# Kernel tuning notes

Measured on AMD Instinct MI355X. Metric: run time of the kernel, lower is better.

Reference implementation:

```python
import jax, jax.numpy as jnp
import numpy as np

B, A = 64, 32            # graphs, atoms per graph
N, E = B * A, B * A * A  # nodes, fully-connected edges (incl. self-loops)
H, LAT = 512, 256        # hidden_dim, latent_dim
L = 4                    # num CSP layers
NF = 10                  # sinusoid frequencies -> dis_dim = 2*NF*3 = 60
MAXA = 100
DIS = 2 * NF * 3
EIN = 2 * H + 9 + DIS    # edge_mlp input width = 1093


def _lin(k, fan_in, shape):
    return jax.random.normal(k, shape, jnp.float32) * (1.0 / np.sqrt(fan_in))


def setup_inputs() -> dict:
    key = jax.random.key(0)
    ks = jax.random.split(key, 20)
    t = jax.random.normal(ks[0], (B, LAT), jnp.float32)
    atom_types = jax.random.randint(ks[1], (N,), 1, MAXA + 1, dtype=jnp.int32)
    frac_coords = jax.random.uniform(ks[2], (N, 3), jnp.float32)
    lattices = jax.random.normal(ks[3], (B, 3, 3), jnp.float32)
    node2graph = jnp.repeat(jnp.arange(B, dtype=jnp.int32), A)
    # fc edges per graph, row-major like dense_to_sparse(block_diag(ones))
    base = (np.arange(B, dtype=np.int64) * A)[:, None]
    ii = np.repeat(np.arange(A), A)
    jj = np.tile(np.arange(A), A)
    src = (base + ii[None, :]).reshape(-1)
    dst = (base + jj[None, :]).reshape(-1)
    edge_index = jnp.asarray(np.stack([src, dst]), dtype=jnp.int32)
    params = dict(
        emb_table=jax.random.normal(ks[4], (MAXA, H), jnp.float32),
        W_latent=_lin(ks[5], H + LAT, (H + LAT, H)), b_latent=jnp.zeros((H,), jnp.float32),
        edge_W1=_lin(ks[6], EIN, (L, EIN, H)), edge_b1=jnp.zeros((L, H), jnp.float32),
        edge_W2=_lin(ks[7], H, (L, H, H)), edge_b2=jnp.zeros((L, H), jnp.float32),
        node_W1=_lin(ks[8], 2 * H, (L, 2 * H, H)), node_b1=jnp.zeros((L, H), jnp.float32),
        node_W2=_lin(ks[9], H, (L, H, H)), node_b2=jnp.zeros((L, H), jnp.float32),
        coord_W=_lin(ks[10], H, (H, 3)),
        lattice_W=_lin(ks[11], H, (H, 9)),
    )
    return dict(t=t, frac_coords=frac_coords, lattices=lattices, **params,
                atom_types=atom_types, node2graph=node2graph, edge_index=edge_index)


def reference(t, frac_coords, lattices, emb_table, W_latent, b_latent,
              edge_W1, edge_b1, edge_W2, edge_b2,
              node_W1, node_b1, node_W2, node_b2,
              coord_W, lattice_W, atom_types, node2graph, edge_index):
    silu = jax.nn.silu
    src, dst = edge_index[0], edge_index[1]
    edge2graph = node2graph[src]
    # gen_edges (fc): frac_diff per edge
    frac_diff = (frac_coords[dst] - frac_coords[src]) % 1.0            # [E,3]
    # SinusoidsEmbedding (same for every layer)
    freqs = 2.0 * jnp.pi * jnp.arange(NF, dtype=jnp.float32)
    fd = (frac_diff[:, :, None] * freqs).reshape(-1, 3 * NF)
    fd_emb = jnp.concatenate([jnp.sin(fd), jnp.cos(fd)], axis=-1)      # [E,60]
    # lattice inner products (ip=True), broadcast to edges
    lat_ip = jnp.einsum('bij,bkj->bik', lattices, lattices).reshape(-1, 9)
    lat_e = lat_ip[edge2graph]                                          # [E,9]
    # node embedding + time conditioning
    nf = emb_table[atom_types - 1]                                      # [N,H]
    nf = jnp.concatenate([nf, t[node2graph]], axis=1) @ W_latent + b_latent
    ones_e = jnp.ones((src.shape[0], 1), nf.dtype)
    for i in range(L):
        hi, hj = nf[src], nf[dst]
        ein = jnp.concatenate([hi, hj, lat_e, fd_emb], axis=1)          # [E,1093]
        ef = silu(silu(ein @ edge_W1[i] + edge_b1[i]) @ edge_W2[i] + edge_b2[i])
        agg = jax.ops.segment_sum(ef, src, num_segments=N)
        deg = jax.ops.segment_sum(ones_e, src, num_segments=N)
        agg = agg / jnp.maximum(deg, 1.0)                               # scatter-mean
        nin = jnp.concatenate([nf, agg], axis=1)                        # [N,2H]
        nf = nf + silu(silu(nin @ node_W1[i] + node_b1[i]) @ node_W2[i] + node_b2[i])
    coord_out = nf @ coord_W                                            # [N,3]
    gf = jax.ops.segment_sum(nf, node2graph, num_segments=B) / A        # graph mean
    lattice_out = (gf @ lattice_W).reshape(-1, 3, 3)
    lattice_out = jnp.einsum('bij,bjk->bik', lattice_out, lattices)     # ip=True
    return (lattice_out, coord_out)
```

## Files before the change

### kernel.cpp

```cpp
#include <hip/hip_runtime.h>
#include <math.h>


typedef short bf16x8 __attribute__((ext_vector_type(8)));
typedef float f32x4 __attribute__((ext_vector_type(4)));

__device__ __forceinline__ float silu_f(float x) {
    float e = __builtin_amdgcn_exp2f(x * -1.44269504088896f);
    return x * __builtin_amdgcn_rcpf(1.0f + e);
}
__device__ __forceinline__ unsigned short f2bf(float x) {
    unsigned int u = __float_as_uint(x);
    u += 0x7fffu + ((u >> 16) & 1u);
    return (unsigned short)(u >> 16);
}
__device__ __forceinline__ unsigned int cvt_pk_bf16(float lo, float hi) {
    unsigned int r;
    asm("v_cvt_pk_bf16_f32 %0, %1, %2" : "=v"(r) : "v"(lo), "v"(hi));
    return r;
}
__device__ __forceinline__ size_t apack_idx(int ng, int m, int c) {
    return ((size_t)(ng*16 + (c >> 5))*64 + (m + 16*((c >> 3) & 3)))*8 + (c & 7);
}

#define NF_OFF    0
#define UP_OFF    (2048*512)
#define VTD_OFF   (2*2048*512)
#define NFP_OFF   (VTD_OFF + 1048576)
#define H1P_OFF   (NFP_OFF + 524288)
#define AGGP_OFF  (H1P_OFF + 524288)
#define WBF_OFF   (AGGP_OFF + 524288)
#define SZ_INITT (512*768)
#define SZ_UVT   (1024*512)
#define SZ_W1DT  (512*64)
#define SZ_W2T   (512*512)
#define SZ_NW1T  (512*1024)
#define SZ_NW2T  (512*512)
#define SZ_LAYER (SZ_UVT+SZ_W1DT+SZ_W2T+SZ_NW1T+SZ_NW2T)
#define WBF_FLOATS ((SZ_INITT + 4*SZ_LAYER + 1)/2)
#define FDP_OFF   (WBF_OFF + WBF_FLOATS)

__global__ __launch_bounds__(256) void k_prep(
    const float* __restrict__ Wl, const float* __restrict__ eW1,
    const float* __restrict__ eW2, const float* __restrict__ nW1,
    const float* __restrict__ nW2, unsigned short* __restrict__ wbf)
{
    __shared__ float tile[32][33];
    int bid = blockIdx.x;
    const float* src; int K; unsigned short* dst; int t;
    if (bid < 384) { src = Wl; K = 768; dst = wbf; t = bid; }
    else {
        int b = bid - 384; int l = b / 1568; int j = b - l * 1568;
        const float* e1 = eW1 + (size_t)l * 1093 * 512;
        unsigned short* base = wbf + SZ_INITT + (size_t)l * SZ_LAYER;
        if (j < 256)      { src = e1;                       K = 512;  dst = base;                                   t = j; }
        else if (j < 512) { src = e1 + 512*512;             K = 512;  dst = base + 512*512;                         t = j-256; }
        else if (j < 544) { src = e1 + 1033*512;            K = 60;   dst = base + SZ_UVT;                          t = j-512; }
        else if (j < 800) { src = eW2 + (size_t)l*512*512;  K = 512;  dst = base + SZ_UVT+SZ_W1DT;                  t = j-544; }
        else if (j <1312) { src = nW1 + (size_t)l*1024*512; K = 1024; dst = base + SZ_UVT+SZ_W1DT+SZ_W2T;           t = j-800; }
        else              { src = nW2 + (size_t)l*512*512;  K = 512;  dst = base + SZ_UVT+SZ_W1DT+SZ_W2T+SZ_NW1T;   t = j-1312; }
    }
    int tr = t >> 4, tc = t & 15;
    int k0 = tr * 32, nn0 = tc * 32;
    {
        int r8 = threadIdx.x >> 5, cc = threadIdx.x & 31;
        #pragma unroll
        for (int rr = 0; rr < 4; ++rr) {
            int row = rr*8 + r8;
            int k = k0 + row;
            tile[row][cc] = (k < K) ? src[(size_t)k*512 + nn0 + cc] : 0.f;
        }
    }
    __syncthreads();
    int nt_loc = threadIdx.x >> 7;
    int l = (threadIdx.x >> 1) & 63;
    int jh = threadIdx.x & 1;
    int lj = l & 15, lh = l >> 4;
    float v0 = tile[lh*8 + jh*4 + 0][nt_loc*16 + lj];
    float v1 = tile[lh*8 + jh*4 + 1][nt_loc*16 + lj];
    float v2 = tile[lh*8 + jh*4 + 2][nt_loc*16 + lj];
    float v3 = tile[lh*8 + jh*4 + 3][nt_loc*16 + lj];
    uint2 pk = { cvt_pk_bf16(v0, v1), cvt_pk_bf16(v2, v3) };
    *(uint2*)&dst[((size_t)(tr*32 + tc*2 + nt_loc)*64 + l)*8 + jh*4] = pk;
}

__global__ __launch_bounds__(64) void k_fd(const float* __restrict__ frac,
                                           unsigned short* __restrict__ fdP)
{
    int bid = blockIdx.x;
    int n0 = bid * 2, g = n0 >> 5;
    int l = threadIdx.x, lj = l & 15, lh = l >> 4;
    float di[2][2][3];
    #pragma unroll
    for (int h = 0; h < 2; ++h)
        #pragma unroll
        for (int dd = 0; dd < 2; ++dd) {
            int dstn = g*32 + dd*16 + lj;
            #pragma unroll
            for (int comp = 0; comp < 3; ++comp) {
                float d = frac[dstn*3 + comp] - frac[(n0+h)*3 + comp];
                d -= floorf(d);
                di[h][dd][comp] = d;
            }
        }
    #pragma unroll
    for (int kt = 0; kt < 2; ++kt)
        #pragma unroll
        for (int mt = 0; mt < 4; ++mt) {
            int h = mt >> 1, dd = mt & 1;
            unsigned int w[4];
            #pragma unroll
            for (int p = 0; p < 4; ++p) {
                float vv[2];
                #pragma unroll
                for (int e = 0; e < 2; ++e) {
                    int k = kt*32 + lh*8 + p*2 + e;
                    float val = 0.f;
                    if (k < 60) {
                        int isCos = k >= 30;
                        int dq = k - (isCos ? 30 : 0);
                        int comp = dq >= 20 ? 2 : (dq >= 10 ? 1 : 0);
                        int f = dq - comp*10;
                        float u = di[h][dd][comp] * (float)f;
                        u -= floorf(u);
                        val = isCos ? __builtin_amdgcn_cosf(u) : __builtin_amdgcn_sinf(u);
                    }
                    vv[e] = val;
                }
                w[p] = cvt_pk_bf16(vv[0], vv[1]);
            }
            uint4 pk = { w[0], w[1], w[2], w[3] };
            *(uint4*)&fdP[(((size_t)bid*8 + kt*4 + mt)*64 + l)*8] = pk;
        }
}

__global__ __launch_bounds__(256) void k_init(
    const float* __restrict__ tvec, const float* __restrict__ emb,
    const unsigned short* __restrict__ WT, const float* __restrict__ bl,
    const int* __restrict__ atom_types, float* __restrict__ nf,
    unsigned short* __restrict__ nfP)
{
    __shared__ __align__(16) unsigned short cat_s[16*768];
    int ng = blockIdx.x >> 1, half = blockIdx.x & 1;
    int n0 = ng * 16, tid = threadIdx.x;
    for (int idx = tid; idx < 16*192; idx += 256) {
        int m = idx / 192, q = idx - m * 192;
        int k4 = q * 4, n = n0 + m;
        float4 v;
        if (k4 < 512) v = *(const float4*)&emb[(size_t)(atom_types[n]-1)*512 + k4];
        else          v = *(const float4*)&tvec[(size_t)(n>>5)*256 + (k4-512)];
        uint2 pk = { cvt_pk_bf16(v.x, v.y), cvt_pk_bf16(v.z, v.w) };
        *(uint2*)&cat_s[m*768 + (k4 ^ ((m&7)<<3))] = pk;
    }
    __syncthreads();
    int w = tid >> 6, l = tid & 63, lj = l & 15, lh = l >> 4;
    f32x4 acc[4];
    #pragma unroll
    for (int nt = 0; nt < 4; ++nt) acc[nt] = (f32x4){0.f,0.f,0.f,0.f};
    for (int kt = 0; kt < 24; ++kt) {
        int k = kt*32 + lh*8;
        bf16x8 a = *(const bf16x8*)&cat_s[lj*768 + (k ^ ((lj&7)<<3))];
        #pragma unroll
        for (int nt = 0; nt < 4; ++nt) {
            bf16x8 b = *(const bf16x8*)&WT[(((size_t)kt*32 + half*16 + w*4 + nt)*64 + l)*8];
            acc[nt] = __builtin_amdgcn_mfma_f32_16x16x32_bf16(a, b, acc[nt], 0, 0, 0);
        }
    }
    #pragma unroll
    for (int nt = 0; nt < 4; ++nt) {
        int c = half*256 + w*64 + nt*16 + lj;
        float bv = bl[c];
        #pragma unroll
        for (int r = 0; r < 4; ++r) {
            int m = lh*4 + r;
            float v = acc[nt][r] + bv;
            nf[(size_t)(n0 + m)*512 + c] = v;
            nfP[apack_idx(ng, m, c)] = f2bf(v);
        }
    }
}

__global__ __launch_bounds__(256) void k_uv(
    const unsigned short* __restrict__ nfP, const unsigned short* __restrict__ WT,
    const float* __restrict__ lat, const float* __restrict__ W1c,
    const float* __restrict__ b1, float* __restrict__ Up,
    float* __restrict__ VTD)
{
    int ng = blockIdx.x >> 2, half = (blockIdx.x >> 1) & 1, ch = blockIdx.x & 1;
    int n0 = ng * 16, g = n0 >> 5, tid = threadIdx.x;
    int w = tid >> 6, l = tid & 63, lj = l & 15, lh = l >> 4;
    const unsigned short* Wh = WT + (size_t)half*512*512;
    f32x4 acc[4];
    #pragma unroll
    for (int nt = 0; nt < 4; ++nt) acc[nt] = (f32x4){0.f,0.f,0.f,0.f};
    bf16x8 acur, anxt, bcur[4], bnxt[4];
    acur = *(const bf16x8*)&nfP[((size_t)(ng*16 + 0)*64 + l)*8];
    #pragma unroll
    for (int nt = 0; nt < 4; ++nt)
        bcur[nt] = *(const bf16x8*)&Wh[(((size_t)0*32 + ch*16 + w*4 + nt)*64 + l)*8];
    for (int kt = 0; kt < 16; ++kt) {
        if (kt < 15) {
            anxt = *(const bf16x8*)&nfP[((size_t)(ng*16 + kt + 1)*64 + l)*8];
            #pragma unroll
            for (int nt = 0; nt < 4; ++nt)
                bnxt[nt] = *(const bf16x8*)&Wh[(((size_t)(kt+1)*32 + ch*16 + w*4 + nt)*64 + l)*8];
        }
        #pragma unroll
        for (int nt = 0; nt < 4; ++nt)
            acc[nt] = __builtin_amdgcn_mfma_f32_16x16x32_bf16(acur, bcur[nt], acc[nt], 0, 0, 0);
        acur = anxt;
        #pragma unroll
        for (int nt = 0; nt < 4; ++nt) bcur[nt] = bnxt[nt];
    }
    if (half == 0) {
        float L[9], lip[9];
        #pragma unroll
        for (int i = 0; i < 9; ++i) L[i] = lat[g*9 + i];
        #pragma unroll
        for (int i = 0; i < 3; ++i)
            #pragma unroll
            for (int kk = 0; kk < 3; ++kk)
                lip[i*3+kk] = L[i*3]*L[kk*3] + L[i*3+1]*L[kk*3+1] + L[i*3+2]*L[kk*3+2];
        #pragma unroll
        for (int nt = 0; nt < 4; ++nt) {
            int c = ch*256 + w*64 + nt*16 + lj;
            float p3 = b1[c];
            #pragma unroll
            for (int t9 = 0; t9 < 9; ++t9) p3 += lip[t9] * W1c[t9*512 + c];
            #pragma unroll
            for (int r = 0; r < 4; ++r)
                Up[(size_t)(n0 + lh*4 + r)*512 + c] = acc[nt][r] + p3;
        }
    } else {
        int dd = (n0 & 31) >> 4;
        #pragma unroll
        for (int nt = 0; nt < 4; ++nt) {
            int ct = ch*16 + w*4 + nt;
            #pragma unroll
            for (int rr = 0; rr < 4; ++rr)
                VTD[(size_t)g*16384 + ct*512 + dd*256 + (lh*4+rr)*16 + lj] = acc[nt][rr];
        }
    }
}

__global__ __launch_bounds__(512) void k_edge(
    const float* __restrict__ Up, const float* __restrict__ VTD,
    const unsigned short* __restrict__ fdP,
    const unsigned short* __restrict__ W1dT,
    const unsigned short* __restrict__ W2T, const float* __restrict__ b2,
    unsigned short* __restrict__ aggP)
{
    __shared__ __align__(16) unsigned short ef1_s[64*512];
    int n0 = blockIdx.x * 2, g = n0 >> 5, tid = threadIdx.x;
    int wid = tid >> 6, l = tid & 63, lj = l & 15, lh = l >> 4;

    {
        bf16x8 fdf[2][4];
        #pragma unroll
        for (int kt = 0; kt < 2; ++kt)
            #pragma unroll
            for (int mt = 0; mt < 4; ++mt)
                fdf[kt][mt] = *(const bf16x8*)&fdP[(((size_t)blockIdx.x*8 + kt*4 + mt)*64 + l)*8];

        #pragma unroll
        for (int q = 0; q < 4; ++q) {
            int ct = wid*4 + q;
            f32x4 a1[4];
            #pragma unroll
            for (int mt = 0; mt < 4; ++mt)
                a1[mt] = *(const f32x4*)&VTD[(size_t)g*16384 + ct*512 + (mt&1)*256 + lj*16 + lh*4];
            #pragma unroll
            for (int kt = 0; kt < 2; ++kt) {
                bf16x8 wf = *(const bf16x8*)&W1dT[(((size_t)kt*32 + ct)*64 + l)*8];
                #pragma unroll
                for (int mt = 0; mt < 4; ++mt)
                    a1[mt] = __builtin_amdgcn_mfma_f32_16x16x32_bf16(wf, fdf[kt][mt], a1[mt], 0, 0, 0);
            }
            int c0 = wid*64 + q*16 + lh*4;
            float4 bs0 = *(const float4*)&Up[(size_t)n0*512 + c0];
            float4 bs1 = *(const float4*)&Up[(size_t)(n0+1)*512 + c0];
            #pragma unroll
            for (int mt = 0; mt < 4; ++mt) {
                float4 bb = (mt >> 1) ? bs1 : bs0;
                int m = mt*16 + lj;
                float x0 = silu_f(a1[mt][0] + bb.x);
                float x1 = silu_f(a1[mt][1] + bb.y);
                float x2 = silu_f(a1[mt][2] + bb.z);
                float x3 = silu_f(a1[mt][3] + bb.w);
                uint2 pk = { cvt_pk_bf16(x0, x1), cvt_pk_bf16(x2, x3) };
                *(uint2*)&ef1_s[m*512 + (c0 ^ ((m&7)<<3))] = pk;
            }
        }
    }
    __syncthreads();

    f32x4 acc2[4][4];
    #pragma unroll
    for (int mt = 0; mt < 4; ++mt)
        #pragma unroll
        for (int nt = 0; nt < 4; ++nt) acc2[mt][nt] = (f32x4){0.f,0.f,0.f,0.f};

    bf16x8 bcur[4], bnxt[4];
    #pragma unroll
    for (int nt = 0; nt < 4; ++nt)
        bcur[nt] = *(const bf16x8*)&W2T[(((size_t)0*32 + wid*4 + nt)*64 + l)*8];

    for (int kt = 0; kt < 16; ++kt) {
        int k = kt*32 + lh*8;
        bf16x8 af[4];
        #pragma unroll
        for (int mt = 0; mt < 4; ++mt) {
            int m = mt*16 + lj;
            af[mt] = *(const bf16x8*)&ef1_s[m*512 + (k ^ ((m&7)<<3))];
        }
        if (kt < 15) {
            #pragma unroll
            for (int nt = 0; nt < 4; ++nt)
                bnxt[nt] = *(const bf16x8*)&W2T[(((size_t)(kt+1)*32 + wid*4 + nt)*64 + l)*8];
        }
        __builtin_amdgcn_s_setprio(1);
        #pragma unroll
        for (int nt = 0; nt < 4; ++nt) {
            #pragma unroll
            for (int mt = 0; mt < 4; ++mt)
                acc2[mt][nt] = __builtin_amdgcn_mfma_f32_16x16x32_bf16(af[mt], bcur[nt], acc2[mt][nt], 0, 0, 0);
        }
        __builtin_amdgcn_s_setprio(0);
        #pragma unroll
        for (int nt = 0; nt < 4; ++nt) bcur[nt] = bnxt[nt];
    }

    int ngg = n0 >> 4, m0 = n0 & 15;
    #pragma unroll
    for (int nt = 0; nt < 4; ++nt) {
        int cc = wid*64 + nt*16 + lj;
        float bv = b2[cc];
        float s0 = 0.f, s1 = 0.f;
        #pragma unroll
        for (int mt = 0; mt < 4; ++mt)
            #pragma unroll
            for (int r = 0; r < 4; ++r) {
                float x = silu_f(acc2[mt][nt][r] + bv);
                if (mt < 2) s0 += x; else s1 += x;
            }
        s0 += __shfl_xor(s0, 16); s0 += __shfl_xor(s0, 32);
        s1 += __shfl_xor(s1, 16); s1 += __shfl_xor(s1, 32);
        if (lh == 0) {
            aggP[apack_idx(ngg, m0,     cc)] = f2bf(s0 * (1.0f/32.0f));
            aggP[apack_idx(ngg, m0 + 1, cc)] = f2bf(s1 * (1.0f/32.0f));
        }
    }
}

__global__ __launch_bounds__(256) void k_node1(
    const unsigned short* __restrict__ nfP, const unsigned short* __restrict__ aggP,
    const unsigned short* __restrict__ W1T, const float* __restrict__ b1,
    unsigned short* __restrict__ h1P)
{
    int ng = blockIdx.x >> 2, cq = blockIdx.x & 3, tid = threadIdx.x;
    int w = tid >> 6, l = tid & 63, lj = l & 15, lh = l >> 4;
    f32x4 acc[2];
    acc[0] = (f32x4){0.f,0.f,0.f,0.f};
    acc[1] = (f32x4){0.f,0.f,0.f,0.f};
    bf16x8 acur, anxt, bcur[2], bnxt[2];
    acur = *(const bf16x8*)&nfP[((size_t)(ng*16 + 0)*64 + l)*8];
    #pragma unroll
    for (int nt = 0; nt < 2; ++nt)
        bcur[nt] = *(const bf16x8*)&W1T[(((size_t)0*32 + cq*8 + w*2 + nt)*64 + l)*8];
    for (int kt = 0; kt < 32; ++kt) {
        if (kt < 31) {
            int kn = kt + 1;
            anxt = (kn < 16)
                ? *(const bf16x8*)&nfP[((size_t)(ng*16 + kn)*64 + l)*8]
                : *(const bf16x8*)&aggP[((size_t)(ng*16 + kn - 16)*64 + l)*8];
            #pragma unroll
            for (int nt = 0; nt < 2; ++nt)
                bnxt[nt] = *(const bf16x8*)&W1T[(((size_t)kn*32 + cq*8 + w*2 + nt)*64 + l)*8];
        }
        #pragma unroll
        for (int nt = 0; nt < 2; ++nt)
            acc[nt] = __builtin_amdgcn_mfma_f32_16x16x32_bf16(acur, bcur[nt], acc[nt], 0, 0, 0);
        acur = anxt;
        #pragma unroll
        for (int nt = 0; nt < 2; ++nt) bcur[nt] = bnxt[nt];
    }
    #pragma unroll
    for (int nt = 0; nt < 2; ++nt) {
        int c = cq*128 + w*32 + nt*16 + lj;
        float bv = b1[c];
        #pragma unroll
        for (int r = 0; r < 4; ++r) {
            int m = lh*4 + r;
            h1P[apack_idx(ng, m, c)] = f2bf(silu_f(acc[nt][r] + bv));
        }
    }
}

__global__ __launch_bounds__(256) void k_node2(
    float* __restrict__ nf, const unsigned short* __restrict__ h1P,
    const unsigned short* __restrict__ W2T, const float* __restrict__ b2,
    unsigned short* __restrict__ nfP)
{
    int ng = blockIdx.x >> 2, cq = blockIdx.x & 3, tid = threadIdx.x;
    int n0 = ng * 16;
    int w = tid >> 6, l = tid & 63, lj = l & 15, lh = l >> 4;
    f32x4 acc[2];
    acc[0] = (f32x4){0.f,0.f,0.f,0.f};
    acc[1] = (f32x4){0.f,0.f,0.f,0.f};
    bf16x8 acur, anxt, bcur[2], bnxt[2];
    acur = *(const bf16x8*)&h1P[((size_t)(ng*16 + 0)*64 + l)*8];
    #pragma unroll
    for (int nt = 0; nt < 2; ++nt)
        bcur[nt] = *(const bf16x8*)&W2T[(((size_t)0*32 + cq*8 + w*2 + nt)*64 + l)*8];
    for (int kt = 0; kt < 16; ++kt) {
        if (kt < 15) {
            anxt = *(const bf16x8*)&h1P[((size_t)(ng*16 + kt + 1)*64 + l)*8];
            #pragma unroll
            for (int nt = 0; nt < 2; ++nt)
                bnxt[nt] = *(const bf16x8*)&W2T[(((size_t)(kt+1)*32 + cq*8 + w*2 + nt)*64 + l)*8];
        }
        #pragma unroll
        for (int nt = 0; nt < 2; ++nt)
            acc[nt] = __builtin_amdgcn_mfma_f32_16x16x32_bf16(acur, bcur[nt], acc[nt], 0, 0, 0);
        acur = anxt;
        #pragma unroll
        for (int nt = 0; nt < 2; ++nt) bcur[nt] = bnxt[nt];
    }
    #pragma unroll
    for (int nt = 0; nt < 2; ++nt) {
        int c = cq*128 + w*32 + nt*16 + lj;
        float bv = b2[c];
        #pragma unroll
        for (int r = 0; r < 4; ++r) {
            int m = lh*4 + r;
            size_t o = (size_t)(n0 + m)*512 + c;
            float v = nf[o] + silu_f(acc[nt][r] + bv);
            nf[o] = v;
            nfP[apack_idx(ng, m, c)] = f2bf(v);
        }
    }
}

__global__ __launch_bounds__(256) void k_coord(const float* __restrict__ nf,
                                               const float* __restrict__ cW,
                                               float* __restrict__ out) {
    int b = blockIdx.x, t = threadIdx.x;
    int nl = t >> 3, s = t & 7;
    int n = b*32 + nl;
    const float* row = nf + (size_t)n*512 + s*64;
    float p0 = 0.f, p1 = 0.f, p2 = 0.f;
    #pragma unroll
    for (int k4 = 0; k4 < 64; k4 += 4) {
        float4 v = *(const float4*)&row[k4];
        int kg = s*64 + k4;
        p0 += v.x*cW[(kg+0)*3+0] + v.y*cW[(kg+1)*3+0] + v.z*cW[(kg+2)*3+0] + v.w*cW[(kg+3)*3+0];
        p1 += v.x*cW[(kg+0)*3+1] + v.y*cW[(kg+1)*3+1] + v.z*cW[(kg+2)*3+1] + v.w*cW[(kg+3)*3+1];
        p2 += v.x*cW[(kg+0)*3+2] + v.y*cW[(kg+1)*3+2] + v.z*cW[(kg+2)*3+2] + v.w*cW[(kg+3)*3+2];
    }
    p0 += __shfl_xor(p0, 1); p0 += __shfl_xor(p0, 2); p0 += __shfl_xor(p0, 4);
    p1 += __shfl_xor(p1, 1); p1 += __shfl_xor(p1, 2); p1 += __shfl_xor(p1, 4);
    p2 += __shfl_xor(p2, 1); p2 += __shfl_xor(p2, 2); p2 += __shfl_xor(p2, 4);
    if (s == 0) {
        out[576 + n*3 + 0] = p0;
        out[576 + n*3 + 1] = p1;
        out[576 + n*3 + 2] = p2;
    }
}

__global__ __launch_bounds__(256) void k_graph(const float* __restrict__ nf,
                                               const float* __restrict__ lW,
                                               const float* __restrict__ lat,
                                               float* __restrict__ out) {
    __shared__ float gf[512];
    __shared__ float lo9[9];
    int b = blockIdx.x, tid = threadIdx.x;
    float s0 = 0.f, s1 = 0.f;
    for (int r = 0; r < 32; ++r) {
        s0 += nf[(b * 32 + r) * 512 + tid];
        s1 += nf[(b * 32 + r) * 512 + tid + 256];
    }
    gf[tid]       = s0 * (1.f / 32.f);
    gf[tid + 256] = s1 * (1.f / 32.f);
    __syncthreads();
    if (tid < 9) {
        float s = 0.f;
        for (int k = 0; k < 512; ++k) s += gf[k] * lW[k * 9 + tid];
        lo9[tid] = s;
    }
    __syncthreads();
    if (tid < 9) {
        int i = tid / 3, kk = tid - (tid / 3) * 3;
        float s = lo9[i*3+0] * lat[b*9 + 0*3 + kk]
                + lo9[i*3+1] * lat[b*9 + 1*3 + kk]
                + lo9[i*3+2] * lat[b*9 + 2*3 + kk];
        out[b * 9 + tid] = s;
    }
}

extern "C" void kernel_launch(void* const* d_in, const int* in_sizes, int n_in,
                              void* d_out, int out_size, void* d_ws, size_t ws_size,
                              hipStream_t stream)
{
    const float* t    = (const float*)d_in[0];
    const float* frac = (const float*)d_in[1];
    const float* lat  = (const float*)d_in[2];
    const float* emb  = (const float*)d_in[3];
    const float* Wl   = (const float*)d_in[4];
    const float* bl   = (const float*)d_in[5];
    const float* eW1  = (const float*)d_in[6];
    const float* eb1  = (const float*)d_in[7];
    const float* eW2  = (const float*)d_in[8];
    const float* eb2  = (const float*)d_in[9];
    const float* nW1  = (const float*)d_in[10];
    const float* nb1  = (const float*)d_in[11];
    const float* nW2  = (const float*)d_in[12];
    const float* nb2  = (const float*)d_in[13];
    const float* cW   = (const float*)d_in[14];
    const float* lW   = (const float*)d_in[15];
    const int* atom_types = (const int*)d_in[16];

    float* out  = (float*)d_out;
    float* wsf  = (float*)d_ws;
    float* nf   = wsf + NF_OFF;
    float* Up   = wsf + UP_OFF;
    float* VTD  = wsf + VTD_OFF;
    unsigned short* nfP  = (unsigned short*)(wsf + NFP_OFF);
    unsigned short* h1P  = (unsigned short*)(wsf + H1P_OFF);
    unsigned short* aggP = (unsigned short*)(wsf + AGGP_OFF);
    unsigned short* wbf  = (unsigned short*)(wsf + WBF_OFF);
    unsigned short* fdP  = (unsigned short*)(wsf + FDP_OFF);

    k_prep<<<384 + 4*1568, 256, 0, stream>>>(Wl, eW1, eW2, nW1, nW2, wbf);
    k_fd<<<1024, 64, 0, stream>>>(frac, fdP);
    k_init<<<256, 256, 0, stream>>>(t, emb, wbf, bl, atom_types, nf, nfP);
    for (int l = 0; l < 4; ++l) {
        const unsigned short* base = wbf + SZ_INITT + (size_t)l * SZ_LAYER;
        const unsigned short* w1dT = base + SZ_UVT;
        const unsigned short* w2T  = w1dT + SZ_W1DT;
        const unsigned short* nw1T = w2T + SZ_W2T;
        const unsigned short* nw2T = nw1T + SZ_NW1T;
        k_uv<<<512, 256, 0, stream>>>(nfP, base, lat,
                                      eW1 + (size_t)l*1093*512 + 1024*512,
                                      eb1 + l*512, Up, VTD);
        k_edge<<<1024, 512, 0, stream>>>(Up, VTD, fdP, w1dT, w2T,
                                         eb2 + l*512, aggP);
        k_node1<<<512, 256, 0, stream>>>(nfP, aggP, nw1T, nb1 + l*512, h1P);
        k_node2<<<512, 256, 0, stream>>>(nf, h1P, nw2T, nb2 + l*512, nfP);
    }
    k_coord<<<64, 256, 0, stream>>>(nf, cW, out);
    k_graph<<<64, 256, 0, stream>>>(nf, lW, lat, out);
}
```

Measured before the change: 355.4 us.

## Split node and UV GEMMs across more blocks and prefetch LDS A-fragments in edge GEMM

The k_uv, k_node1 and k_node2 kernels now launch twice as many blocks, each computing half as many output column tiles per wave. This raises parallelism for these small skinny GEMMs on a GPU with many CUs, at the cost of rereading the A operand more times. Separately, the second GEMM in k_edge double-buffers its LDS A-fragment loads one k-step ahead so they can overlap with the MFMAs, which uses more registers.

```diff
diff --git a/kernel.cpp b/kernel.cpp
--- a/kernel.cpp
+++ b/kernel.cpp
@@ -186,31 +186,31 @@
     const float* __restrict__ b1, float* __restrict__ Up,
     float* __restrict__ VTD)
 {
-    int ng = blockIdx.x >> 2, half = (blockIdx.x >> 1) & 1, ch = blockIdx.x & 1;
+    int ng = blockIdx.x >> 3, half = (blockIdx.x >> 2) & 1, chq = blockIdx.x & 3;
     int n0 = ng * 16, g = n0 >> 5, tid = threadIdx.x;
     int w = tid >> 6, l = tid & 63, lj = l & 15, lh = l >> 4;
     const unsigned short* Wh = WT + (size_t)half*512*512;
-    f32x4 acc[4];
-    #pragma unroll
-    for (int nt = 0; nt < 4; ++nt) acc[nt] = (f32x4){0.f,0.f,0.f,0.f};
-    bf16x8 acur, anxt, bcur[4], bnxt[4];
+    f32x4 acc[2];
+    acc[0] = (f32x4){0.f,0.f,0.f,0.f};
+    acc[1] = (f32x4){0.f,0.f,0.f,0.f};
+    bf16x8 acur, anxt, bcur[2], bnxt[2];
     acur = *(const bf16x8*)&nfP[((size_t)(ng*16 + 0)*64 + l)*8];
     #pragma unroll
-    for (int nt = 0; nt < 4; ++nt)
-        bcur[nt] = *(const bf16x8*)&Wh[(((size_t)0*32 + ch*16 + w*4 + nt)*64 + l)*8];
+    for (int nt = 0; nt < 2; ++nt)
+        bcur[nt] = *(const bf16x8*)&Wh[(((size_t)0*32 + chq*8 + w*2 + nt)*64 + l)*8];
     for (int kt = 0; kt < 16; ++kt) {
         if (kt < 15) {
             anxt = *(const bf16x8*)&nfP[((size_t)(ng*16 + kt + 1)*64 + l)*8];
             #pragma unroll
-            for (int nt = 0; nt < 4; ++nt)
-                bnxt[nt] = *(const bf16x8*)&Wh[(((size_t)(kt+1)*32 + ch*16 + w*4 + nt)*64 + l)*8];
-        }
-        #pragma unroll
-        for (int nt = 0; nt < 4; ++nt)
+            for (int nt = 0; nt < 2; ++nt)
+                bnxt[nt] = *(const bf16x8*)&Wh[(((size_t)(kt+1)*32 + chq*8 + w*2 + nt)*64 + l)*8];
+        }
+        #pragma unroll
+        for (int nt = 0; nt < 2; ++nt)
             acc[nt] = __builtin_amdgcn_mfma_f32_16x16x32_bf16(acur, bcur[nt], acc[nt], 0, 0, 0);
         acur = anxt;
         #pragma unroll
-        for (int nt = 0; nt < 4; ++nt) bcur[nt] = bnxt[nt];
+        for (int nt = 0; nt < 2; ++nt) bcur[nt] = bnxt[nt];
     }
     if (half == 0) {
         float L[9], lip[9];
@@ -222,8 +222,8 @@
             for (int kk = 0; kk < 3; ++kk)
                 lip[i*3+kk] = L[i*3]*L[kk*3] + L[i*3+1]*L[kk*3+1] + L[i*3+2]*L[kk*3+2];
         #pragma unroll
-        for (int nt = 0; nt < 4; ++nt) {
-            int c = ch*256 + w*64 + nt*16 + lj;
+        for (int nt = 0; nt < 2; ++nt) {
+            int c = chq*128 + w*32 + nt*16 + lj;
             float p3 = b1[c];
             #pragma unroll
             for (int t9 = 0; t9 < 9; ++t9) p3 += lip[t9] * W1c[t9*512 + c];
@@ -234,8 +234,8 @@
     } else {
         int dd = (n0 & 31) >> 4;
         #pragma unroll
-        for (int nt = 0; nt < 4; ++nt) {
-            int ct = ch*16 + w*4 + nt;
+        for (int nt = 0; nt < 2; ++nt) {
+            int ct = chq*8 + w*2 + nt;
             #pragma unroll
             for (int rr = 0; rr < 4; ++rr)
                 VTD[(size_t)g*16384 + ct*512 + dd*256 + (lh*4+rr)*16 + lj] = acc[nt][rr];
@@ -300,20 +300,24 @@
         #pragma unroll
         for (int nt = 0; nt < 4; ++nt) acc2[mt][nt] = (f32x4){0.f,0.f,0.f,0.f};
 
-    bf16x8 bcur[4], bnxt[4];
+    bf16x8 bcur[4], bnxt[4], afc[4], afn[4];
     #pragma unroll
     for (int nt = 0; nt < 4; ++nt)
         bcur[nt] = *(const bf16x8*)&W2T[(((size_t)0*32 + wid*4 + nt)*64 + l)*8];
+    #pragma unroll
+    for (int mt = 0; mt < 4; ++mt) {
+        int m = mt*16 + lj;
+        afc[mt] = *(const bf16x8*)&ef1_s[m*512 + ((lh*8) ^ ((m&7)<<3))];
+    }
 
     for (int kt = 0; kt < 16; ++kt) {
-        int k = kt*32 + lh*8;
-        bf16x8 af[4];
-        #pragma unroll
-        for (int mt = 0; mt < 4; ++mt) {
-            int m = mt*16 + lj;
-            af[mt] = *(const bf16x8*)&ef1_s[m*512 + (k ^ ((m&7)<<3))];
-        }
         if (kt < 15) {
+            int kn = (kt+1)*32 + lh*8;
+            #pragma unroll
+            for (int mt = 0; mt < 4; ++mt) {
+                int m = mt*16 + lj;
+                afn[mt] = *(const bf16x8*)&ef1_s[m*512 + (kn ^ ((m&7)<<3))];
+            }
             #pragma unroll
             for (int nt = 0; nt < 4; ++nt)
                 bnxt[nt] = *(const bf16x8*)&W2T[(((size_t)(kt+1)*32 + wid*4 + nt)*64 + l)*8];
@@ -323,9 +327,11 @@
         for (int nt = 0; nt < 4; ++nt) {
             #pragma unroll
             for (int mt = 0; mt < 4; ++mt)
-                acc2[mt][nt] = __builtin_amdgcn_mfma_f32_16x16x32_bf16(af[mt], bcur[nt], acc2[mt][nt], 0, 0, 0);
+                acc2[mt][nt] = __builtin_amdgcn_mfma_f32_16x16x32_bf16(afc[mt], bcur[nt], acc2[mt][nt], 0, 0, 0);
         }
         __builtin_amdgcn_s_setprio(0);
+        #pragma unroll
+        for (int mt = 0; mt < 4; ++mt) afc[mt] = afn[mt];
         #pragma unroll
         for (int nt = 0; nt < 4; ++nt) bcur[nt] = bnxt[nt];
     }
@@ -357,42 +363,30 @@
     const unsigned short* __restrict__ W1T, const float* __restrict__ b1,
     unsigned short* __restrict__ h1P)
 {
-    int ng = blockIdx.x >> 2, cq = blockIdx.x & 3, tid = threadIdx.x;
+    int ng = blockIdx.x >> 3, cq = blockIdx.x & 7, tid = threadIdx.x;
     int w = tid >> 6, l = tid & 63, lj = l & 15, lh = l >> 4;
-    f32x4 acc[2];
-    acc[0] = (f32x4){0.f,0.f,0.f,0.f};
-    acc[1] = (f32x4){0.f,0.f,0.f,0.f};
-    bf16x8 acur, anxt, bcur[2], bnxt[2];
+    f32x4 acc = (f32x4){0.f,0.f,0.f,0.f};
+    bf16x8 acur, anxt, bcur, bnxt;
     acur = *(const bf16x8*)&nfP[((size_t)(ng*16 + 0)*64 + l)*8];
-    #pragma unroll
-    for (int nt = 0; nt < 2; ++nt)
-        bcur[nt] = *(const bf16x8*)&W1T[(((size_t)0*32 + cq*8 + w*2 + nt)*64 + l)*8];
+    bcur = *(const bf16x8*)&W1T[(((size_t)0*32 + cq*4 + w)*64 + l)*8];
     for (int kt = 0; kt < 32; ++kt) {
         if (kt < 31) {
             int kn = kt + 1;
             anxt = (kn < 16)
                 ? *(const bf16x8*)&nfP[((size_t)(ng*16 + kn)*64 + l)*8]
                 : *(const bf16x8*)&aggP[((size_t)(ng*16 + kn - 16)*64 + l)*8];
-            #pragma unroll
-            for (int nt = 0; nt < 2; ++nt)
-                bnxt[nt] = *(const bf16x8*)&W1T[(((size_t)kn*32 + cq*8 + w*2 + nt)*64 + l)*8];
-        }
-        #pragma unroll
-        for (int nt = 0; nt < 2; ++nt)
-            acc[nt] = __builtin_amdgcn_mfma_f32_16x16x32_bf16(acur, bcur[nt], acc[nt], 0, 0, 0);
+            bnxt = *(const bf16x8*)&W1T[(((size_t)kn*32 + cq*4 + w)*64 + l)*8];
+        }
+        acc = __builtin_amdgcn_mfma_f32_16x16x32_bf16(acur, bcur, acc, 0, 0, 0);
         acur = anxt;
-        #pragma unroll
-        for (int nt = 0; nt < 2; ++nt) bcur[nt] = bnxt[nt];
-    }
-    #pragma unroll
-    for (int nt = 0; nt < 2; ++nt) {
-        int c = cq*128 + w*32 + nt*16 + lj;
-        float bv = b1[c];
-        #pragma unroll
-        for (int r = 0; r < 4; ++r) {
-            int m = lh*4 + r;
-            h1P[apack_idx(ng, m, c)] = f2bf(silu_f(acc[nt][r] + bv));
-        }
+        bcur = bnxt;
+    }
+    int c = cq*64 + w*16 + lj;
+    float bv = b1[c];
+    #pragma unroll
+    for (int r = 0; r < 4; ++r) {
+        int m = lh*4 + r;
+        h1P[apack_idx(ng, m, c)] = f2bf(silu_f(acc[r] + bv));
     }
 }
 
@@ -401,43 +395,31 @@
     const unsigned short* __restrict__ W2T, const float* __restrict__ b2,
     unsigned short* __restrict__ nfP)
 {
-    int ng = blockIdx.x >> 2, cq = blockIdx.x & 3, tid = threadIdx.x;
+    int ng = blockIdx.x >> 3, cq = blockIdx.x & 7, tid = threadIdx.x;
     int n0 = ng * 16;
     int w = tid >> 6, l = tid & 63, lj = l & 15, lh = l >> 4;
-    f32x4 acc[2];
-    acc[0] = (f32x4){0.f,0.f,0.f,0.f};
-    acc[1] = (f32x4){0.f,0.f,0.f,0.f};
-    bf16x8 acur, anxt, bcur[2], bnxt[2];
+    f32x4 acc = (f32x4){0.f,0.f,0.f,0.f};
+    bf16x8 acur, anxt, bcur, bnxt;
     acur = *(const bf16x8*)&h1P[((size_t)(ng*16 + 0)*64 + l)*8];
-    #pragma unroll
-    for (int nt = 0; nt < 2; ++nt)
-        bcur[nt] = *(const bf16x8*)&W2T[(((size_t)0*32 + cq*8 + w*2 + nt)*64 + l)*8];
+    bcur = *(const bf16x8*)&W2T[(((size_t)0*32 + cq*4 + w)*64 + l)*8];
     for (int kt = 0; kt < 16; ++kt) {
         if (kt < 15) {
             anxt = *(const bf16x8*)&h1P[((size_t)(ng*16 + kt + 1)*64 + l)*8];
-            #pragma unroll
-            for (int nt = 0; nt < 2; ++nt)
-                bnxt[nt] = *(const bf16x8*)&W2T[(((size_t)(kt+1)*32 + cq*8 + w*2 + nt)*64 + l)*8];
-        }
-        #pragma unroll
-        for (int nt = 0; nt < 2; ++nt)
-            acc[nt] = __builtin_amdgcn_mfma_f32_16x16x32_bf16(acur, bcur[nt], acc[nt], 0, 0, 0);
+            bnxt = *(const bf16x8*)&W2T[(((size_t)(kt+1)*32 + cq*4 + w)*64 + l)*8];
+        }
+        acc = __builtin_amdgcn_mfma_f32_16x16x32_bf16(acur, bcur, acc, 0, 0, 0);
         acur = anxt;
-        #pragma unroll
-        for (int nt = 0; nt < 2; ++nt) bcur[nt] = bnxt[nt];
-    }
-    #pragma unroll
-    for (int nt = 0; nt < 2; ++nt) {
-        int c = cq*128 + w*32 + nt*16 + lj;
-        float bv = b2[c];
-        #pragma unroll
-        for (int r = 0; r < 4; ++r) {
-            int m = lh*4 + r;
-            size_t o = (size_t)(n0 + m)*512 + c;
-            float v = nf[o] + silu_f(acc[nt][r] + bv);
-            nf[o] = v;
-            nfP[apack_idx(ng, m, c)] = f2bf(v);
-        }
+        bcur = bnxt;
+    }
+    int c = cq*64 + w*16 + lj;
+    float bv = b2[c];
+    #pragma unroll
+    for (int r = 0; r < 4; ++r) {
+        int m = lh*4 + r;
+        size_t o = (size_t)(n0 + m)*512 + c;
+        float v = nf[o] + silu_f(acc[r] + bv);
+        nf[o] = v;
+        nfP[apack_idx(ng, m, c)] = f2bf(v);
     }
 }
 
@@ -539,13 +521,13 @@
         const unsigned short* w2T  = w1dT + SZ_W1DT;
         const unsigned short* nw1T = w2T + SZ_W2T;
         const unsigned short* nw2T = nw1T + SZ_NW1T;
-        k_uv<<<512, 256, 0, stream>>>(nfP, base, lat,
-                                      eW1 + (size_t)l*1093*512 + 1024*512,
-                                      eb1 + l*512, Up, VTD);
+        k_uv<<<1024, 256, 0, stream>>>(nfP, base, lat,
+                                       eW1 + (size_t)l*1093*512 + 1024*512,
+                                       eb1 + l*512, Up, VTD);
         k_edge<<<1024, 512, 0, stream>>>(Up, VTD, fdP, w1dT, w2T,
                                          eb2 + l*512, aggP);
-        k_node1<<<512, 256, 0, stream>>>(nfP, aggP, nw1T, nb1 + l*512, h1P);
-        k_node2<<<512, 256, 0, stream>>>(nf, h1P, nw2T, nb2 + l*512, nfP);
+        k_node1<<<1024, 256, 0, stream>>>(nfP, aggP, nw1T, nb1 + l*512, h1P);
+        k_node2<<<1024, 256, 0, stream>>>(nf, h1P, nw2T, nb2 + l*512, nfP);
     }
     k_coord<<<64, 256, 0, stream>>>(nf, cW, out);
     k_graph<<<64, 256, 0, stream>>>(nf, lW, lat, out);
```

Measured after the change: 354.3 us. Within noise of the previous version (-0.3%).
